# Kernel optimization log

Hardware: AMD Instinct MI355X
Metric: run time of the kernel (lower is better)

## Reference

```python
import jax, jax.numpy as jnp
import numpy as np

B, S, D = 2, 4096, 512
H = 8
HD = D // H


def setup_inputs() -> dict:
    key = jax.random.key(0)
    k1, k2, k3, k4, k5 = jax.random.split(key, 5)
    sd = 1.0 / np.sqrt(D)
    return {
        "x": jax.random.normal(k1, (B, S, D), dtype=jnp.float32),
        "Wqkv": jax.random.normal(k2, (3 * D, D), dtype=jnp.float32) * sd,
        "bqkv": jax.random.normal(k3, (3 * D,), dtype=jnp.float32) * 0.02,
        "Wo": jax.random.normal(k4, (D, D), dtype=jnp.float32) * sd,
        "bo": jax.random.normal(k5, (D,), dtype=jnp.float32) * 0.02,
    }


def reference(x, Wqkv, bqkv, Wo, bo):
    b, s, d = x.shape
    h, hd = H, d // H
    # QKV projection (torch Linear: x @ W^T + b)
    qkv = x @ Wqkv.T + bqkv                      # [b, s, 3d]
    q, k, v = jnp.split(qkv, 3, axis=-1)         # each [b, s, d]
    # [b, s, h, hd] -> [b, h, s, hd]
    q = q.reshape(b, s, h, hd).transpose(0, 2, 1, 3)
    k = k.reshape(b, s, h, hd).transpose(0, 2, 1, 3)
    v = v.reshape(b, s, h, hd).transpose(0, 2, 1, 3)
    # causal additive mask: triu(ones, diag=1) * -1e10
    mask = jnp.triu(jnp.ones((s, s), dtype=x.dtype), k=1) * jnp.asarray(-1e10, x.dtype)
    wts = jnp.einsum("bhqd,bhkd->bhqk", q, k) / np.sqrt(hd).astype(np.float32)
    wts = wts + mask[None, None, :, :]
    wts = jax.nn.softmax(wts, axis=-1)
    y = jnp.einsum("bhqk,bhkd->bhqd", wts, v)    # [b, h, s, hd]
    y = y.transpose(0, 2, 1, 3).reshape(b, s, d) # [b, s, d]
    out = y @ Wo.T + bo
    return out
```

## Files before the change

kernel.cpp:

```cpp
#include <hip/hip_runtime.h>


typedef __bf16 bf16x8 __attribute__((ext_vector_type(8)));
typedef float f32x4 __attribute__((ext_vector_type(4)));
typedef unsigned short u16;

#define MFMA(a, b, c) __builtin_amdgcn_mfma_f32_16x16x32_bf16(a, b, c, 0, 0, 0)
#define QSCALE 0.18033688011112042f
#define FIXEDM 12.0f

__device__ __forceinline__ float exp2_fast(float x) {
    return __builtin_amdgcn_exp2f(x);
}
__device__ __forceinline__ u16 f2bf(float f) {
    union { __bf16 h; u16 u; } v; v.h = (__bf16)f; return v.u;
}
__device__ __forceinline__ ushort4 f4_to_bf4(float4 v) {
    ushort4 r;
    r.x = f2bf(v.x); r.y = f2bf(v.y); r.z = f2bf(v.z); r.w = f2bf(v.w);
    return r;
}
__device__ __forceinline__ void load_lds16(const u16* g, u16* l) {
    __builtin_amdgcn_global_load_lds(
        (const __attribute__((address_space(1))) void*)g,
        (__attribute__((address_space(3))) void*)l, 16, 0, 0);
}

__global__ __launch_bounds__(256) void cvt_all(
    const float* __restrict__ x, const float* __restrict__ wq,
    const float* __restrict__ wo,
    u16* __restrict__ xb, u16* __restrict__ wqb, u16* __restrict__ wob)
{
    int i = blockIdx.x * 256 + threadIdx.x;
    if (i < 1048576) {
        ((ushort4*)xb)[i] = f4_to_bf4(((const float4*)x)[i]);
    } else if (i < 1048576 + 196608) {
        int j = i - 1048576;
        ((ushort4*)wqb)[j] = f4_to_bf4(((const float4*)wq)[j]);
    } else {
        int j = i - 1048576 - 196608;
        ((ushort4*)wob)[j] = f4_to_bf4(((const float4*)wo)[j]);
    }
}

__global__ __launch_bounds__(256) void gemm_qkv_bf(
    const u16* __restrict__ X, const u16* __restrict__ W,
    const float* __restrict__ bias,
    u16* __restrict__ QY, u16* __restrict__ Ko, u16* __restrict__ Vto)
{
    __shared__ u16 As[128 * 32];
    __shared__ u16 Bs[128 * 32];
    const int K = 512;
    const int tid = threadIdx.x, wave = tid >> 6, lane = tid & 63;
    const int l15 = lane & 15, quad = lane >> 4;
    const int bm = blockIdx.x * 128, bn = blockIdx.y * 128;
    const int wr = wave >> 1, wc = wave & 1;
    const int arow = lane >> 2;
    const int acol = (lane & 3) * 8;

    f32x4 acc[4][4] = {};
    for (int k0 = 0; k0 < K; k0 += 32) {
        __syncthreads();
#pragma unroll
        for (int ii = 0; ii < 2; ii++) {
            const int inst = wave * 2 + ii;
            const int row = inst * 16 + arow;
            load_lds16(&X[(bm + row) * K + k0 + acol], &As[inst * 512]);
            load_lds16(&W[(bn + row) * K + k0 + acol], &Bs[inst * 512]);
        }
        __syncthreads();
        bf16x8 a[4], b[4];
#pragma unroll
        for (int i = 0; i < 4; i++)
            a[i] = *(const bf16x8*)&As[(wr * 64 + i * 16 + l15) * 32 + quad * 8];
#pragma unroll
        for (int j = 0; j < 4; j++)
            b[j] = *(const bf16x8*)&Bs[(wc * 64 + j * 16 + l15) * 32 + quad * 8];
#pragma unroll
        for (int i = 0; i < 4; i++)
#pragma unroll
            for (int j = 0; j < 4; j++)
                acc[i][j] = MFMA(b[i], a[j], acc[i][j]);
    }

    const int nbase = bn + wc * 64;
    const int which = nbase >> 9;
#pragma unroll
    for (int i = 0; i < 4; i++) {
        const int d0 = nbase + i * 16 + quad * 4;
        const float4 bv = *(const float4*)&bias[d0];
        const int d0m = d0 & 511;
        const int h = d0m >> 6, hd0 = d0m & 63;
#pragma unroll
        for (int j = 0; j < 4; j++) {
            const int s_g = bm + wr * 64 + j * 16 + l15;
            const int b_ = s_g >> 12, s0 = s_g & 4095;
            const int bhh = b_ * 8 + h;
            if (which == 2) {
#pragma unroll
                for (int r = 0; r < 4; r++) {
                    const float bvr = (r == 0) ? bv.x : (r == 1) ? bv.y : (r == 2) ? bv.z : bv.w;
                    Vto[((size_t)(bhh * 64 + hd0 + r)) * 4096 + s0] = f2bf(acc[i][j][r] + bvr);
                }
            } else if (which == 1) {
                ushort4 pk;
                pk.x = f2bf(acc[i][j][0] + bv.x);
                pk.y = f2bf(acc[i][j][1] + bv.y);
                pk.z = f2bf(acc[i][j][2] + bv.z);
                pk.w = f2bf(acc[i][j][3] + bv.w);
                *(ushort4*)&Ko[(bhh * 4096 + s0) * 64 + hd0] = pk;
            } else {
                ushort4 pk;
                pk.x = f2bf((acc[i][j][0] + bv.x) * QSCALE);
                pk.y = f2bf((acc[i][j][1] + bv.y) * QSCALE);
                pk.z = f2bf((acc[i][j][2] + bv.z) * QSCALE);
                pk.w = f2bf((acc[i][j][3] + bv.w) * QSCALE);
                *(ushort4*)&QY[((b_ * 4096 + s0) * 8 + h) * 64 + hd0] = pk;
            }
        }
    }
}

#define LS 72

__global__ __launch_bounds__(256, 4) void attn_k(
    const u16* __restrict__ QY, const u16* __restrict__ Kk, const u16* __restrict__ Vt,
    u16* __restrict__ PO, float* __restrict__ ML)
{
    __shared__ u16 Ks[64 * LS];
    __shared__ u16 Vs[64 * LS];
    __shared__ u16 Ps[4 * 16 * LS];

    const int tid = threadIdx.x, wave = tid >> 6, lane = tid & 63;
    const int l15 = lane & 15, quad = lane >> 4;
    const int bh = blockIdx.x;
    const int b_ = bh >> 3, h = bh & 7;
    const int xi = (int)blockIdx.y;
    const int qt = 31 - (xi >> 1);
    const int seg = xi & 1;
    const int half = qt + 1;
    const int kt0 = seg ? half : 0;
    const int kt1 = seg ? 2 * qt + 2 : half;
    const int base_r = qt * 128 + wave * 32;

    const u16* qpa = &QY[((b_ * 4096 + base_r + l15) * 8 + h) * 64];
    const u16* qpb = qpa + 16 * 8 * 64;
    bf16x8 qa0 = *(const bf16x8*)&qpa[quad * 8];
    bf16x8 qa1 = *(const bf16x8*)&qpa[32 + quad * 8];
    bf16x8 qb0 = *(const bf16x8*)&qpb[quad * 8];
    bf16x8 qb1 = *(const bf16x8*)&qpb[32 + quad * 8];

    f32x4 oa[4] = {}, ob[4] = {};
    float la = 0.0f, lb = 0.0f;

    const int srow = tid >> 2;
    const int scol = (tid & 3) * 16;
    const u16* Kg = &Kk[(bh * 4096 + srow) * 64 + scol];
    const u16* Vg = &Vt[(bh * 64 + srow) * 4096 + scol];

    bf16x8 pk0 = *(const bf16x8*)&Kg[kt0 * 4096];
    bf16x8 pk1 = *(const bf16x8*)&Kg[kt0 * 4096 + 8];
    bf16x8 pv0 = *(const bf16x8*)&Vg[kt0 * 64];
    bf16x8 pv1 = *(const bf16x8*)&Vg[kt0 * 64 + 8];

    u16* P = &Ps[wave * 16 * LS];

    for (int kt = kt0; kt < kt1; kt++) {
        const int k0 = kt * 64;
        __syncthreads();
        *(bf16x8*)&Ks[srow * LS + scol] = pk0;
        *(bf16x8*)&Ks[srow * LS + scol + 8] = pk1;
        *(bf16x8*)&Vs[srow * LS + scol] = pv0;
        *(bf16x8*)&Vs[srow * LS + scol + 8] = pv1;
        if (kt + 1 < kt1) {
            pk0 = *(const bf16x8*)&Kg[(kt + 1) * 4096];
            pk1 = *(const bf16x8*)&Kg[(kt + 1) * 4096 + 8];
            pv0 = *(const bf16x8*)&Vg[(kt + 1) * 64];
            pv1 = *(const bf16x8*)&Vg[(kt + 1) * 64 + 8];
        }
        __syncthreads();

        f32x4 sa[4], sb[4];
#pragma unroll
        for (int j = 0; j < 4; j++) {
            const int krow = j * 16 + l15;
            bf16x8 kf0 = *(const bf16x8*)&Ks[krow * LS + quad * 8];
            bf16x8 kf1 = *(const bf16x8*)&Ks[krow * LS + 32 + quad * 8];
            f32x4 s = {};
            s = MFMA(kf0, qa0, s);
            s = MFMA(kf1, qa1, s);
            sa[j] = s;
            f32x4 t = {};
            t = MFMA(kf0, qb0, t);
            t = MFMA(kf1, qb1, t);
            sb[j] = t;
        }

        {
            const bool needmask = (k0 + 63 > base_r);
            float spa[4][4];
#pragma unroll
            for (int j = 0; j < 4; j++)
#pragma unroll
                for (int r = 0; r < 4; r++) {
                    float v = sa[j][r];
                    if (needmask) {
                        const int key = k0 + j * 16 + quad * 4 + r;
                        if (key > base_r + l15) v = -1e30f;
                    }
                    const float p = exp2_fast(v - FIXEDM);
                    spa[j][r] = p;
                    la += p;
                }
#pragma unroll
            for (int j = 0; j < 4; j++) {
                ushort4 w;
                w.x = f2bf(spa[j][0]); w.y = f2bf(spa[j][1]);
                w.z = f2bf(spa[j][2]); w.w = f2bf(spa[j][3]);
                *(ushort4*)&P[l15 * LS + j * 16 + quad * 4] = w;
            }
        }

        float spb[4][4];
        {
            const bool needmask = (k0 + 63 > base_r + 16);
#pragma unroll
            for (int j = 0; j < 4; j++)
#pragma unroll
                for (int r = 0; r < 4; r++) {
                    float v = sb[j][r];
                    if (needmask) {
                        const int key = k0 + j * 16 + quad * 4 + r;
                        if (key > base_r + 16 + l15) v = -1e30f;
                    }
                    const float p = exp2_fast(v - FIXEDM);
                    spb[j][r] = p;
                    lb += p;
                }
        }

        bf16x8 pfa0 = *(const bf16x8*)&P[l15 * LS + quad * 8];
        bf16x8 pfa1 = *(const bf16x8*)&P[l15 * LS + 32 + quad * 8];
#pragma unroll
        for (int j = 0; j < 4; j++) {
            ushort4 w;
            w.x = f2bf(spb[j][0]); w.y = f2bf(spb[j][1]);
            w.z = f2bf(spb[j][2]); w.w = f2bf(spb[j][3]);
            *(ushort4*)&P[l15 * LS + j * 16 + quad * 4] = w;
        }
        bf16x8 pfb0 = *(const bf16x8*)&P[l15 * LS + quad * 8];
        bf16x8 pfb1 = *(const bf16x8*)&P[l15 * LS + 32 + quad * 8];

#pragma unroll
        for (int n = 0; n < 4; n++) {
            const int vrow = n * 16 + l15;
            bf16x8 vf0 = *(const bf16x8*)&Vs[vrow * LS + quad * 8];
            bf16x8 vf1 = *(const bf16x8*)&Vs[vrow * LS + 32 + quad * 8];
            oa[n] = MFMA(vf0, pfa0, oa[n]);
            oa[n] = MFMA(vf1, pfa1, oa[n]);
            ob[n] = MFMA(vf0, pfb0, ob[n]);
            ob[n] = MFMA(vf1, pfb1, ob[n]);
        }
    }

    float lfa = la;
    lfa += __shfl_xor(lfa, 16);
    lfa += __shfl_xor(lfa, 32);
    float lfb = lb;
    lfb += __shfl_xor(lfb, 16);
    lfb += __shfl_xor(lfb, 32);
    const float iva = (lfa > 0.0f) ? 1.0f / lfa : 0.0f;
    const float ivb = (lfb > 0.0f) ? 1.0f / lfb : 0.0f;
    u16* ppa = &PO[(size_t)seg * 4194304 +
                   (size_t)((b_ * 4096 + base_r + l15) * 8 + h) * 64];
    u16* ppb = ppa + 16 * 8 * 64;
#pragma unroll
    for (int n = 0; n < 4; n++) {
        ushort4 wa;
        wa.x = f2bf(oa[n][0] * iva);
        wa.y = f2bf(oa[n][1] * iva);
        wa.z = f2bf(oa[n][2] * iva);
        wa.w = f2bf(oa[n][3] * iva);
        *(ushort4*)&ppa[n * 16 + quad * 4] = wa;
        ushort4 wb;
        wb.x = f2bf(ob[n][0] * ivb);
        wb.y = f2bf(ob[n][1] * ivb);
        wb.z = f2bf(ob[n][2] * ivb);
        wb.w = f2bf(ob[n][3] * ivb);
        *(ushort4*)&ppb[n * 16 + quad * 4] = wb;
    }
    if (quad == 0) {
        float* mpa = &ML[((seg * 16 + bh) * 4096 + base_r + l15) * 2];
        mpa[0] = FIXEDM;
        mpa[1] = lfa;
        float* mpb = mpa + 16 * 2;
        mpb[0] = FIXEDM;
        mpb[1] = lfb;
    }
}

__global__ __launch_bounds__(256) void merge_k(
    const u16* __restrict__ PO, const float* __restrict__ ML, u16* __restrict__ Y)
{
    const int flat = blockIdx.x * 256 + threadIdx.x;
    const int rs = flat >> 6;
    const int rem = flat & 63;
    const int h = rem >> 3, c = rem & 7;
    const int b_ = rs >> 12, s = rs & 4095;
    const int bh = b_ * 8 + h;
    const float m0 = ML[(bh * 4096 + s) * 2];
    const float l0 = ML[(bh * 4096 + s) * 2 + 1];
    const float m1 = ML[((16 + bh) * 4096 + s) * 2];
    const float l1 = ML[((16 + bh) * 4096 + s) * 2 + 1];
    const float m = fmaxf(m0, m1);
    const float w0 = (l0 > 0.0f) ? exp2_fast(m0 - m) * l0 : 0.0f;
    const float w1 = (l1 > 0.0f) ? exp2_fast(m1 - m) * l1 : 0.0f;
    const float inv = 1.0f / (w0 + w1);
    const float a0 = w0 * inv, a1 = w1 * inv;

    const size_t base = (size_t)(rs * 8 + h) * 64 + c * 8;
    bf16x8 x0 = *(const bf16x8*)&PO[base];
    bf16x8 x1 = *(const bf16x8*)&PO[4194304 + base];
    ushort4 lo, hi;
    lo.x = f2bf(a0 * (float)x0[0] + a1 * (float)x1[0]);
    lo.y = f2bf(a0 * (float)x0[1] + a1 * (float)x1[1]);
    lo.z = f2bf(a0 * (float)x0[2] + a1 * (float)x1[2]);
    lo.w = f2bf(a0 * (float)x0[3] + a1 * (float)x1[3]);
    hi.x = f2bf(a0 * (float)x0[4] + a1 * (float)x1[4]);
    hi.y = f2bf(a0 * (float)x0[5] + a1 * (float)x1[5]);
    hi.z = f2bf(a0 * (float)x0[6] + a1 * (float)x1[6]);
    hi.w = f2bf(a0 * (float)x0[7] + a1 * (float)x1[7]);
    *(ushort4*)&Y[base] = lo;
    *(ushort4*)&Y[base + 4] = hi;
}

__global__ __launch_bounds__(256) void gemm_o_bf(
    const u16* __restrict__ X, const u16* __restrict__ W,
    const float* __restrict__ bias, float* __restrict__ Out)
{
    __shared__ u16 As[128 * 32];
    __shared__ u16 Bs[128 * 32];
    const int K = 512;
    const int tid = threadIdx.x, wave = tid >> 6, lane = tid & 63;
    const int l15 = lane & 15, quad = lane >> 4;
    const int bm = blockIdx.x * 128, bn = blockIdx.y * 128;
    const int wr = wave >> 1, wc = wave & 1;
    const int arow = lane >> 2;
    const int acol = (lane & 3) * 8;

    f32x4 acc[4][4] = {};
    for (int k0 = 0; k0 < K; k0 += 32) {
        __syncthreads();
#pragma unroll
        for (int ii = 0; ii < 2; ii++) {
            const int inst = wave * 2 + ii;
            const int row = inst * 16 + arow;
            load_lds16(&X[(bm + row) * K + k0 + acol], &As[inst * 512]);
            load_lds16(&W[(bn + row) * K + k0 + acol], &Bs[inst * 512]);
        }
        __syncthreads();
        bf16x8 a[4], b[4];
#pragma unroll
        for (int i = 0; i < 4; i++)
            a[i] = *(const bf16x8*)&As[(wr * 64 + i * 16 + l15) * 32 + quad * 8];
#pragma unroll
        for (int j = 0; j < 4; j++)
            b[j] = *(const bf16x8*)&Bs[(wc * 64 + j * 16 + l15) * 32 + quad * 8];
#pragma unroll
        for (int i = 0; i < 4; i++)
#pragma unroll
            for (int j = 0; j < 4; j++)
                acc[i][j] = MFMA(b[i], a[j], acc[i][j]);
    }
#pragma unroll
    for (int i = 0; i < 4; i++) {
        const int n0 = bn + wc * 64 + i * 16 + quad * 4;
        const float4 bv = *(const float4*)&bias[n0];
#pragma unroll
        for (int j = 0; j < 4; j++) {
            const int m = bm + wr * 64 + j * 16 + l15;
            float4 ov;
            ov.x = acc[i][j][0] + bv.x;
            ov.y = acc[i][j][1] + bv.y;
            ov.z = acc[i][j][2] + bv.z;
            ov.w = acc[i][j][3] + bv.w;
            *(float4*)&Out[(size_t)m * 512 + n0] = ov;
        }
    }
}

extern "C" void kernel_launch(void* const* d_in, const int* in_sizes, int n_in,
                              void* d_out, int out_size, void* d_ws, size_t ws_size,
                              hipStream_t stream) {
    (void)in_sizes; (void)n_in; (void)out_size; (void)ws_size;
    const float* x    = (const float*)d_in[0];
    const float* Wqkv = (const float*)d_in[1];
    const float* bqkv = (const float*)d_in[2];
    const float* Wo   = (const float*)d_in[3];
    const float* bo   = (const float*)d_in[4];
    float* out = (float*)d_out;

    u16* qy_ws = (u16*)d_ws;
    u16* k_ws  = qy_ws + 4194304;
    u16* vt_ws = k_ws + 4194304;
    float* ml  = (float*)(vt_ws + 4194304);
    u16* wqkvb = (u16*)(ml + 262144);
    u16* wob   = wqkvb + 786432;
    u16* xb    = (u16*)d_out;
    u16* po    = (u16*)d_out;

    cvt_all<<<5120, 256, 0, stream>>>(x, Wqkv, Wo, xb, wqkvb, wob);
    gemm_qkv_bf<<<dim3(64, 12), 256, 0, stream>>>(xb, wqkvb, bqkv, qy_ws, k_ws, vt_ws);
    attn_k<<<dim3(16, 64), 256, 0, stream>>>(qy_ws, k_ws, vt_ws, po, ml);
    merge_k<<<2048, 256, 0, stream>>>(po, ml, qy_ws);
    gemm_o_bf<<<dim3(64, 4), 256, 0, stream>>>(qy_ws, wob, bo, out);
}
```

Measured before the change: 199.4 us.

## Use direct global-to-LDS loads with XOR swizzle, MFMA row sums, reordered tiles

Replaces the register-staged K/V prefetch with global_load_lds direct copies into an XOR-swizzled unpadded LDS layout, which removes the VGPR staging and LDS store instructions. Softmax row sums are now computed with an MFMA against a ones vector instead of scalar adds plus shuffles, taking VALU work off the exp path. Block-to-query-tile mapping is changed to a serpentine layered order to balance causal work across CUs. The cost is that the next tile is no longer prefetched while the current one computes, so load latency is exposed between the barriers.

```diff
diff --git a/kernel.cpp b/kernel.cpp
--- a/kernel.cpp
+++ b/kernel.cpp
@@ -127,20 +127,21 @@
     const u16* __restrict__ QY, const u16* __restrict__ Kk, const u16* __restrict__ Vt,
     u16* __restrict__ PO, float* __restrict__ ML)
 {
-    __shared__ u16 Ks[64 * LS];
-    __shared__ u16 Vs[64 * LS];
+    __shared__ u16 Ks[64 * 64];
+    __shared__ u16 Vs[64 * 64];
     __shared__ u16 Ps[4 * 16 * LS];
 
     const int tid = threadIdx.x, wave = tid >> 6, lane = tid & 63;
     const int l15 = lane & 15, quad = lane >> 4;
     const int bh = blockIdx.x;
     const int b_ = bh >> 3, h = bh & 7;
-    const int xi = (int)blockIdx.y;
-    const int qt = 31 - (xi >> 1);
-    const int seg = xi & 1;
-    const int half = qt + 1;
-    const int kt0 = seg ? half : 0;
-    const int kt1 = seg ? 2 * qt + 2 : half;
+    const int u = (int)blockIdx.y;
+    const int layer = u >> 4;
+    const int p = u & 15;
+    const int pp = p >> 1, seg = p & 1;
+    const int qt = layer * 8 + ((layer & 1) ? (7 - pp) : pp);
+    const int kt0 = seg ? (qt + 1) : 0;
+    const int kt1 = seg ? (2 * qt + 2) : (qt + 1);
     const int base_r = qt * 128 + wave * 32;
 
     const u16* qpa = &QY[((b_ * 4096 + base_r + l15) * 8 + h) * 64];
@@ -151,41 +152,40 @@
     bf16x8 qb1 = *(const bf16x8*)&qpb[32 + quad * 8];
 
     f32x4 oa[4] = {}, ob[4] = {};
-    float la = 0.0f, lb = 0.0f;
-
-    const int srow = tid >> 2;
-    const int scol = (tid & 3) * 16;
-    const u16* Kg = &Kk[(bh * 4096 + srow) * 64 + scol];
-    const u16* Vg = &Vt[(bh * 64 + srow) * 4096 + scol];
-
-    bf16x8 pk0 = *(const bf16x8*)&Kg[kt0 * 4096];
-    bf16x8 pk1 = *(const bf16x8*)&Kg[kt0 * 4096 + 8];
-    bf16x8 pv0 = *(const bf16x8*)&Vg[kt0 * 64];
-    bf16x8 pv1 = *(const bf16x8*)&Vg[kt0 * 64 + 8];
+    f32x4 lacc_a = {}, lacc_b = {};
+
+    const int r0 = tid >> 3;
+    const int swz = 8 * ((tid & 7) ^ (r0 & 7));
+    const u16* KgA = &Kk[(size_t)bh * 4096 * 64 + r0 * 64 + swz];
+    const u16* VgA = &Vt[(size_t)bh * 64 * 4096 + r0 * 4096 + swz];
+    u16* ldsK0 = &Ks[wave * 512];
+    u16* ldsK1 = &Ks[wave * 512 + 2048];
+    u16* ldsV0 = &Vs[wave * 512];
+    u16* ldsV1 = &Vs[wave * 512 + 2048];
+
+    const int c0 = 8 * (quad ^ (l15 & 7));
+
+    bf16x8 ones;
+#pragma unroll
+    for (int i = 0; i < 8; i++) ones[i] = (__bf16)1.0f;
 
     u16* P = &Ps[wave * 16 * LS];
 
     for (int kt = kt0; kt < kt1; kt++) {
         const int k0 = kt * 64;
         __syncthreads();
-        *(bf16x8*)&Ks[srow * LS + scol] = pk0;
-        *(bf16x8*)&Ks[srow * LS + scol + 8] = pk1;
-        *(bf16x8*)&Vs[srow * LS + scol] = pv0;
-        *(bf16x8*)&Vs[srow * LS + scol + 8] = pv1;
-        if (kt + 1 < kt1) {
-            pk0 = *(const bf16x8*)&Kg[(kt + 1) * 4096];
-            pk1 = *(const bf16x8*)&Kg[(kt + 1) * 4096 + 8];
-            pv0 = *(const bf16x8*)&Vg[(kt + 1) * 64];
-            pv1 = *(const bf16x8*)&Vg[(kt + 1) * 64 + 8];
-        }
+        load_lds16(KgA + kt * 4096, ldsK0);
+        load_lds16(KgA + kt * 4096 + 2048, ldsK1);
+        load_lds16(VgA + k0, ldsV0);
+        load_lds16(VgA + k0 + 131072, ldsV1);
         __syncthreads();
 
         f32x4 sa[4], sb[4];
 #pragma unroll
         for (int j = 0; j < 4; j++) {
-            const int krow = j * 16 + l15;
-            bf16x8 kf0 = *(const bf16x8*)&Ks[krow * LS + quad * 8];
-            bf16x8 kf1 = *(const bf16x8*)&Ks[krow * LS + 32 + quad * 8];
+            const int kb = (j * 16 + l15) * 64;
+            bf16x8 kf0 = *(const bf16x8*)&Ks[kb + c0];
+            bf16x8 kf1 = *(const bf16x8*)&Ks[kb + (c0 ^ 32)];
             f32x4 s = {};
             s = MFMA(kf0, qa0, s);
             s = MFMA(kf1, qa1, s);
@@ -208,9 +208,7 @@
                         const int key = k0 + j * 16 + quad * 4 + r;
                         if (key > base_r + l15) v = -1e30f;
                     }
-                    const float p = exp2_fast(v - FIXEDM);
-                    spa[j][r] = p;
-                    la += p;
+                    spa[j][r] = exp2_fast(v - FIXEDM);
                 }
 #pragma unroll
             for (int j = 0; j < 4; j++) {
@@ -233,9 +231,7 @@
                         const int key = k0 + j * 16 + quad * 4 + r;
                         if (key > base_r + 16 + l15) v = -1e30f;
                     }
-                    const float p = exp2_fast(v - FIXEDM);
-                    spb[j][r] = p;
-                    lb += p;
+                    spb[j][r] = exp2_fast(v - FIXEDM);
                 }
         }
 
@@ -251,11 +247,16 @@
         bf16x8 pfb0 = *(const bf16x8*)&P[l15 * LS + quad * 8];
         bf16x8 pfb1 = *(const bf16x8*)&P[l15 * LS + 32 + quad * 8];
 
+        lacc_a = MFMA(ones, pfa0, lacc_a);
+        lacc_a = MFMA(ones, pfa1, lacc_a);
+        lacc_b = MFMA(ones, pfb0, lacc_b);
+        lacc_b = MFMA(ones, pfb1, lacc_b);
+
 #pragma unroll
         for (int n = 0; n < 4; n++) {
-            const int vrow = n * 16 + l15;
-            bf16x8 vf0 = *(const bf16x8*)&Vs[vrow * LS + quad * 8];
-            bf16x8 vf1 = *(const bf16x8*)&Vs[vrow * LS + 32 + quad * 8];
+            const int vb = (n * 16 + l15) * 64;
+            bf16x8 vf0 = *(const bf16x8*)&Vs[vb + c0];
+            bf16x8 vf1 = *(const bf16x8*)&Vs[vb + (c0 ^ 32)];
             oa[n] = MFMA(vf0, pfa0, oa[n]);
             oa[n] = MFMA(vf1, pfa1, oa[n]);
             ob[n] = MFMA(vf0, pfb0, ob[n]);
@@ -263,12 +264,8 @@
         }
     }
 
-    float lfa = la;
-    lfa += __shfl_xor(lfa, 16);
-    lfa += __shfl_xor(lfa, 32);
-    float lfb = lb;
-    lfb += __shfl_xor(lfb, 16);
-    lfb += __shfl_xor(lfb, 32);
+    const float lfa = lacc_a[0];
+    const float lfb = lacc_b[0];
     const float iva = (lfa > 0.0f) ? 1.0f / lfa : 0.0f;
     const float ivb = (lfb > 0.0f) ? 1.0f / lfb : 0.0f;
     u16* ppa = &PO[(size_t)seg * 4194304 +
```

After: 195.2 us. 2.1% less time.
